# Kernel tuning notes

Measured on AMD Instinct MI355X. Metric: run time of the kernel, lower is better.

Reference implementation:

```python
import jax, jax.numpy as jnp
import numpy as np

B, T, V, S_FIXED, DIM, CV = 4, 256, 1024, 64, 1024, 256


def setup_inputs() -> dict:
    key = jax.random.key(0)
    ks = jax.random.split(key, 8)
    x = jax.random.normal(ks[0], (B, T, DIM), jnp.float32)
    vision = jax.random.normal(ks[1], (B, V, CV), jnp.float32)
    # attention mask (B, V, T): each text token t attends to exactly S_FIXED vision tokens
    scores = jax.random.uniform(ks[2], (B, T, V))
    _, sel = jax.lax.top_k(scores, S_FIXED)  # (B, T, S)
    mask_tv = jnp.zeros((B, T, V), bool)
    mask_tv = mask_tv.at[jnp.arange(B)[:, None, None], jnp.arange(T)[None, :, None], sel].set(True)
    attention_mask = jnp.transpose(mask_tv, (0, 2, 1))  # (B, V, T)
    # xavier-uniform-like params (scale irrelevant for correctness baseline)
    Wu = jax.random.normal(ks[3], (CV, DIM), jnp.float32) * (1.0 / np.sqrt(CV))
    bu = jax.random.normal(ks[4], (DIM,), jnp.float32) * 0.02
    Wk = jax.random.normal(ks[5], (DIM, DIM), jnp.float32) * (1.0 / np.sqrt(DIM))
    Wv = jax.random.normal(ks[6], (DIM, DIM), jnp.float32) * (1.0 / np.sqrt(DIM))
    return {"x": x, "vision": vision, "attention_mask": attention_mask,
            "Wu": Wu, "bu": bu, "Wk": Wk, "Wv": Wv, "S": S_FIXED}


def reference(x, vision, attention_mask, Wu, bu, Wk, Wv, S):
    Bv, Vn, Cv = vision.shape
    Bx, Tn, C = x.shape  # C == dim
    # --- _construct_sparse_inputs ---
    mask_tv = jnp.transpose(attention_mask, (0, 2, 1))  # (B, T, V)
    idx_full = jnp.where(mask_tv, jnp.arange(Vn, dtype=jnp.int32), jnp.int32(Vn))
    # topk(largest=False) == smallest S indices, ascending; pad value = Vn
    index = -jax.lax.top_k(-idx_full, S)[0]  # (B, T, S)
    vision_pad = jnp.concatenate([vision, jnp.zeros((Bv, 1, Cv), vision.dtype)], axis=1)  # (B, V+1, Cv)
    vg = jnp.take_along_axis(vision_pad, index.reshape(Bv, Tn * S, 1), axis=1)
    vg = vg.reshape(Bv, Tn, S, Cv)  # (B, T, S, 256)
    # NOTE: faithful to source — VALID positions receive the -100 bias
    mask_qk = (index != Vn)[..., None].astype(jnp.float32) * (-100.0)  # (B, T, S, 1)
    # --- attention ---
    vu = vg @ Wu + bu           # (B, T, S, dim)
    k = vu @ Wk                 # (B, T, S, dim)
    v = vu @ Wv                 # (B, T, S, dim)
    q = x[:, :, None, :]        # (B, T, 1, dim)
    qk = jnp.einsum('bksc,bktc->bkst', k, q) / jnp.sqrt(jnp.float32(C)) + mask_qk  # (B, T, S, 1)
    sm = jax.nn.softmax(qk.reshape(Bx, -1), axis=-1).reshape(qk.shape)  # softmax over flattened T*S*1
    attn = jnp.einsum('bkst,bksc->bktc', sm, v)  # (B, T, 1, dim)
    return (attn + q).squeeze(2)  # (B, T, dim)
```

## Files before the change

### kernel.cpp

```cpp
#include <hip/hip_runtime.h>
#include <stdint.h>

#define B 4
#define T 256
#define V 1024
#define S 64
#define DIM 1024
#define CV 256

typedef __attribute__((ext_vector_type(8))) short bf16x8;
typedef __attribute__((ext_vector_type(4))) short s16x4;
typedef __attribute__((ext_vector_type(4))) float f32x4;

enum : int {
    WKT_O   = 0,
    WVT_O   = WKT_O + 262144,
    WUB_O   = WVT_O + 262144,
    WKPB_O  = WUB_O + 131072,
    WVPT_O  = WKPB_O + 131072,
    XB_O    = WVPT_O + 131072,
    ZB_O    = XB_O + 262144,
    VB_O    = ZB_O + 131072,
    WB_O    = VB_O + 524288,
    RS_O    = WB_O + 131072,
    PIDX_O  = RS_O + B*T,
    BK_O    = PIDX_O + B*T*S,
    BV_O    = BK_O + DIM,
    BP_O    = BV_O + DIM,
    WS_TOTAL= BP_O + 2*16*1024
};

__device__ __forceinline__ short f2bf(float f) {
    union { float f; unsigned u; } x; x.f = f;
    unsigned r = (x.u + 0x7FFF + ((x.u >> 16) & 1)) >> 16;
    return (short)r;
}
__device__ __forceinline__ float bf2f(short s) {
    union { unsigned u; float f; } x;
    x.u = ((unsigned)(unsigned short)s) << 16;
    return x.f;
}
__device__ __forceinline__ s16x4 cvt4(float4 f) {
    s16x4 o;
    o.x = f2bf(f.x); o.y = f2bf(f.y); o.z = f2bf(f.z); o.w = f2bf(f.w);
    return o;
}

__global__ void stage1(const float* __restrict__ vision, const float* __restrict__ Wu,
                       const float* __restrict__ x, const float* __restrict__ Wk,
                       const float* __restrict__ Wv, const float* __restrict__ bu,
                       const void* __restrict__ maskp,
                       float* __restrict__ ws, int* __restrict__ wsi) {
    __shared__ short tlds[64 * 65];
    __shared__ float tred[4 * 64];
    __shared__ int mc_cnt[16][17];
    __shared__ int sa_flag, sb_flag;
    int blk = blockIdx.x;
    int tid = threadIdx.x;

    if (blk < 2304) {
        const float* src; short* dst; int idx;
        if (blk < 1024)      { src = vision; dst = (short*)(ws + VB_O);  idx = blk; }
        else if (blk < 1280) { src = Wu;     dst = (short*)(ws + WUB_O); idx = blk - 1024; }
        else                 { src = x;      dst = (short*)(ws + XB_O);  idx = blk - 1280; }
        int i = (idx * 256 + tid);
        ((s16x4*)dst)[i] = cvt4(((const float4*)src)[i]);
        return;
    }
    if (blk < 2816) {
        int tile = blk - 2304;
        int which = tile >> 8, t2 = tile & 255;
        int e0 = (t2 >> 4) * 64, d0 = (t2 & 15) * 64;
        const float* src = which ? Wv : Wk;
        short* dst = (short*)(ws + (which ? WVT_O : WKT_O));
        int j = tid & 63, i0 = tid >> 6;
        float pb = 0.f;
#pragma unroll
        for (int p = 0; p < 16; p++) {
            int i = p * 4 + i0;
            float v = src[(size_t)(e0 + i) * DIM + d0 + j];
            tlds[j * 65 + i] = f2bf(v);
            pb += bu[e0 + i] * v;
        }
        tred[i0 * 64 + j] = pb;
        __syncthreads();
#pragma unroll
        for (int p = 0; p < 16; p++) {
            int dd = p * 4 + i0;
            dst[(size_t)(d0 + dd) * DIM + e0 + j] = tlds[dd * 65 + j];
        }
        if (i0 == 0) {
            float s = tred[j] + tred[64 + j] + tred[128 + j] + tred[192 + j];
            ws[BP_O + (which * 16 + (e0 >> 6)) * 1024 + d0 + j] = s;
        }
        return;
    }
    {
        int a = 0, bfl = 0;
        const uchar4* m4 = (const uchar4*)maskp;
#pragma unroll
        for (int jj = 0; jj < 4; jj++) {
            uchar4 u = m4[tid * 4 + jj];
            if (u.y | u.z | u.w) a = 1;
            if (u.x == 0x3f || u.y == 0x3f || u.z == 0x3f || u.w == 0x3f) bfl = 1;
        }
        if (tid == 0) { sa_flag = 0; sb_flag = 0; }
        __syncthreads();
        if (a) sa_flag = 1;
        if (bfl) sb_flag = 1;
        __syncthreads();
    }
    bool byteMode = sa_flag && !sb_flag;
    int mb = blk - 2816;
    int b = mb >> 4, tg = mb & 15;
    int tl = tid & 15, c = tid >> 4;
    int t = tg * 16 + tl;
    int v0 = c * 64;
    unsigned long long bits = 0ull;
    if (byteMode) {
        const uint8_t* m = (const uint8_t*)maskp + (size_t)(b * V + v0) * T + t;
#pragma unroll 8
        for (int j = 0; j < 64; j++)
            if (m[(size_t)j * T] != 0) bits |= 1ull << j;
    } else {
        const int* m = (const int*)maskp + (size_t)(b * V + v0) * T + t;
#pragma unroll 8
        for (int j = 0; j < 64; j++)
            if (m[(size_t)j * T] != 0) bits |= 1ull << j;
    }
    mc_cnt[tl][c] = __popcll(bits);
    __syncthreads();
    int off = 0, total = 0;
#pragma unroll
    for (int cc = 0; cc < 16; cc++) {
        int cn = mc_cnt[tl][cc];
        if (cc < c) off += cn;
        total += cn;
    }
    int base = PIDX_O + (b * T + t) * S;
    while (bits) {
        int j = __ffsll(bits) - 1;
        bits &= bits - 1;
        if (off < S) wsi[base + off] = v0 + j;
        off++;
    }
    if (c == 15)
        for (int j = (total < S ? total : S); j < S; j++) wsi[base + j] = 0;
}

template<int K, int LDA, int LDB>
__device__ __forceinline__ void wave_mma(const short* __restrict__ A0,
                                         const short* __restrict__ B0,
                                         f32x4 acc[2][2]) {
    int lane = threadIdx.x & 63;
    int rw = lane & 15, q = lane >> 4;
    const short* ap0 = A0 + rw * LDA + q * 8;
    const short* ap1 = ap0 + 16 * LDA;
    const short* bp0 = B0 + rw * LDB + q * 8;
    const short* bp1 = bp0 + 16 * LDB;
#pragma unroll 4
    for (int kc = 0; kc < K; kc += 32) {
        bf16x8 a0 = *(const bf16x8*)(ap0 + kc);
        bf16x8 a1 = *(const bf16x8*)(ap1 + kc);
        bf16x8 b0 = *(const bf16x8*)(bp0 + kc);
        bf16x8 b1 = *(const bf16x8*)(bp1 + kc);
        acc[0][0] = __builtin_amdgcn_mfma_f32_16x16x32_bf16(a0, b0, acc[0][0], 0, 0, 0);
        acc[0][1] = __builtin_amdgcn_mfma_f32_16x16x32_bf16(a0, b1, acc[0][1], 0, 0, 0);
        acc[1][0] = __builtin_amdgcn_mfma_f32_16x16x32_bf16(a1, b0, acc[1][0], 0, 0, 0);
        acc[1][1] = __builtin_amdgcn_mfma_f32_16x16x32_bf16(a1, b1, acc[1][1], 0, 0, 0);
    }
}

__device__ __forceinline__ bool splitk_reduce(f32x4 acc[2][2],
                                              float (*red)[64][17],
                                              int wv, int lane) {
    if (wv > 0) {
#pragma unroll
        for (int i = 0; i < 2; i++)
#pragma unroll
            for (int j = 0; j < 2; j++)
#pragma unroll
                for (int r = 0; r < 4; r++)
                    red[wv - 1][lane][(i * 2 + j) * 4 + r] = acc[i][j][r];
    }
    __syncthreads();
    if (wv != 0) return false;
#pragma unroll
    for (int i = 0; i < 2; i++)
#pragma unroll
        for (int j = 0; j < 2; j++)
#pragma unroll
            for (int r = 0; r < 4; r++) {
                int c = (i * 2 + j) * 4 + r;
                acc[i][j][r] += red[0][lane][c] + red[1][lane][c] + red[2][lane][c];
            }
    return true;
}

__global__ void g_prep_mfma(float* __restrict__ ws) {
    if (blockIdx.x >= 512) {
        int which = blockIdx.x - 512;
#pragma unroll
        for (int cch = 0; cch < 4; cch++) {
            int d = cch * 256 + threadIdx.x;
            float s = 0.f;
#pragma unroll
            for (int g = 0; g < 16; g++)
                s += ws[BP_O + (which * 16 + g) * 1024 + d];
            ws[(which ? BV_O : BK_O) + d] = s;
        }
        return;
    }
    __shared__ float red[3][64][17];
    int tile = blockIdx.x;
    int which = tile >> 8, rem = tile & 255;
    int m0 = (rem >> 5) * 32, n0 = (rem & 31) * 32;
    int wv = threadIdx.x >> 6, lane = threadIdx.x & 63;
    const short* A = (const short*)(ws + WUB_O) + (size_t)m0 * DIM + wv * 256;
    const short* Bt = (const short*)(ws + (which ? WVT_O : WKT_O)) + (size_t)n0 * DIM + wv * 256;
    f32x4 acc[2][2] = {};
    wave_mma<256, DIM, DIM>(A, Bt, acc);
    if (!splitk_reduce(acc, red, wv, lane)) return;
    int col = lane & 15, q = lane >> 4;
    if (which == 0) {
        short* o = (short*)(ws + WKPB_O);
#pragma unroll
        for (int i = 0; i < 2; i++)
#pragma unroll
            for (int j = 0; j < 2; j++)
#pragma unroll
                for (int r = 0; r < 4; r++)
                    o[(size_t)(m0 + i * 16 + q * 4 + r) * DIM + n0 + j * 16 + col] =
                        f2bf(acc[i][j][r]);
    } else {
        short* o = (short*)(ws + WVPT_O);
#pragma unroll
        for (int i = 0; i < 2; i++)
#pragma unroll
            for (int j = 0; j < 2; j++) {
                s16x4 v;
                v.x = f2bf(acc[i][j][0]); v.y = f2bf(acc[i][j][1]);
                v.z = f2bf(acc[i][j][2]); v.w = f2bf(acc[i][j][3]);
                *(s16x4*)&o[(size_t)(n0 + j * 16 + col) * CV + m0 + i * 16 + q * 4] = v;
            }
    }
}

__global__ void g_z_mfma(float* __restrict__ ws) {
    __shared__ float red[3][64][17];
    int w = blockIdx.x;
    int m0 = (w >> 3) * 32, n0 = (w & 7) * 32;
    int wv = threadIdx.x >> 6, lane = threadIdx.x & 63;
    const short* A = (const short*)(ws + XB_O) + (size_t)m0 * DIM + wv * 256;
    const short* Bt = (const short*)(ws + WKPB_O) + (size_t)n0 * DIM + wv * 256;
    f32x4 acc[2][2] = {};
    wave_mma<256, DIM, DIM>(A, Bt, acc);
    if (!splitk_reduce(acc, red, wv, lane)) return;
    int col = lane & 15, q = lane >> 4;
    short* zb = (short*)(ws + ZB_O);
#pragma unroll
    for (int i = 0; i < 2; i++)
#pragma unroll
        for (int j = 0; j < 2; j++)
#pragma unroll
            for (int r = 0; r < 4; r++)
                zb[(size_t)(m0 + i * 16 + q * 4 + r) * CV + n0 + j * 16 + col] =
                    f2bf(acc[i][j][r]);
}

__global__ void __launch_bounds__(256, 4)
g_attn(const float* __restrict__ x, float* __restrict__ ws,
       int* __restrict__ wsi) {
    __shared__ short svr[64 * 256];
    __shared__ int   s_idx[64];
    __shared__ float s_sc[64];
    __shared__ float s_c0[4];
    __shared__ float s_wa[3][64][5];
    int tid = threadIdx.x;
    int lane = tid & 63, wv = tid >> 6;
    int blk = blockIdx.x;
    int bt = ((blk & 7) << 7) + (blk >> 3);
    int b = bt >> 8;

    if (tid < 64) s_idx[tid] = wsi[PIDX_O + bt * S + tid];
    {
        const float4* xr = (const float4*)(x + (size_t)bt * DIM);
        const float4* bkr = (const float4*)(ws + BK_O);
        float4 a = xr[wv * 64 + lane], k4 = bkr[wv * 64 + lane];
        float c0p = a.x * k4.x + a.y * k4.y + a.z * k4.z + a.w * k4.w;
        for (int o = 32; o > 0; o >>= 1) c0p += __shfl_xor(c0p, o);
        if (lane == 0) s_c0[wv] = c0p;
    }
    __syncthreads();
    const short* vb = (const short*)(ws + VB_O) + (size_t)b * V * CV;
    {
        int r = tid >> 2, part = tid & 3;
        const bf16x8* src = (const bf16x8*)(vb + (size_t)s_idx[r] * CV);
#pragma unroll
        for (int i = 0; i < 8; i++) {
            int c = part * 8 + i;
            int sl = c ^ (r & 7);
            *(bf16x8*)((char*)svr + r * 512 + sl * 16) = src[c];
        }
    }
    __syncthreads();
    int rw = lane & 15, q = lane >> 4;
    {
        const short* zp = (const short*)(ws + ZB_O) + (size_t)bt * CV + q * 8;
        int srow = wv * 16 + rw;
        f32x4 a4 = {0.f, 0.f, 0.f, 0.f};
#pragma unroll
        for (int kc8 = 0; kc8 < 8; kc8++) {
            int sl = (q + kc8 * 4) ^ (srow & 7);
            bf16x8 av = *(const bf16x8*)((char*)svr + srow * 512 + sl * 16);
            bf16x8 bv = *(const bf16x8*)(zp + kc8 * 32);
            a4 = __builtin_amdgcn_mfma_f32_16x16x32_bf16(av, bv, a4, 0, 0, 0);
        }
        if (rw == 0) {
#pragma unroll
            for (int r = 0; r < 4; r++)
                s_sc[wv * 16 + q * 4 + r] = a4[r];
        }
    }
    __syncthreads();
    float c0 = s_c0[0] + s_c0[1] + s_c0[2] + s_c0[3];
    float p = expf((s_sc[lane] + c0) * 0.03125f);
    float rs = p;
    for (int o = 32; o > 0; o >>= 1) rs += __shfl_xor(rs, o);
    if (tid == 0) ws[RS_O + bt] = rs;
    float4 wa = {0.f, 0.f, 0.f, 0.f};
#pragma unroll
    for (int si = 0; si < 16; si++) {
        int s = wv * 16 + si;
        float pv = __shfl(p, s);
        int sl = (lane >> 1) ^ (s & 7);
        s16x4 r4 = *(const s16x4*)((char*)svr + s * 512 + sl * 16 + (lane & 1) * 8);
        wa.x += pv * bf2f(r4.x); wa.y += pv * bf2f(r4.y);
        wa.z += pv * bf2f(r4.z); wa.w += pv * bf2f(r4.w);
    }
    if (wv > 0) {
        s_wa[wv - 1][lane][0] = wa.x; s_wa[wv - 1][lane][1] = wa.y;
        s_wa[wv - 1][lane][2] = wa.z; s_wa[wv - 1][lane][3] = wa.w;
    }
    __syncthreads();
    if (wv == 0) {
#pragma unroll
        for (int g = 0; g < 3; g++) {
            wa.x += s_wa[g][lane][0]; wa.y += s_wa[g][lane][1];
            wa.z += s_wa[g][lane][2]; wa.w += s_wa[g][lane][3];
        }
        s16x4 o;
        o.x = f2bf(wa.x); o.y = f2bf(wa.y); o.z = f2bf(wa.z); o.w = f2bf(wa.w);
        ((s16x4*)((short*)(ws + WB_O) + (size_t)bt * CV))[lane] = o;
    }
}

__global__ void g_out_mfma(const float* __restrict__ x, float* __restrict__ ws,
                           float* __restrict__ out) {
    int w = blockIdx.x * 4 + (threadIdx.x >> 6);
    int m0 = (w >> 6) * 32, n0 = (w & 63) * 16;
    int lane = threadIdx.x & 63;
    int b = m0 >> 8;
    float4 r4 = *(const float4*)(ws + RS_O + b * 256 + lane * 4);
    float dn = r4.x + r4.y + r4.z + r4.w;
    for (int o = 32; o > 0; o >>= 1) dn += __shfl_xor(dn, o);
    float inv = 1.0f / dn;
    int rw = lane & 15, q = lane >> 4;
    const short* A  = (const short*)(ws + WB_O)   + (size_t)m0 * CV;
    const short* Bt = (const short*)(ws + WVPT_O) + (size_t)n0 * CV;
    const short* ap0 = A + rw * CV + q * 8;
    const short* ap1 = ap0 + 16 * CV;
    const short* bp0 = Bt + rw * CV + q * 8;
    f32x4 acc[2] = {};
#pragma unroll 4
    for (int kc = 0; kc < CV; kc += 32) {
        bf16x8 a0 = *(const bf16x8*)(ap0 + kc);
        bf16x8 a1 = *(const bf16x8*)(ap1 + kc);
        bf16x8 b0 = *(const bf16x8*)(bp0 + kc);
        acc[0] = __builtin_amdgcn_mfma_f32_16x16x32_bf16(a0, b0, acc[0], 0, 0, 0);
        acc[1] = __builtin_amdgcn_mfma_f32_16x16x32_bf16(a1, b0, acc[1], 0, 0, 0);
    }
    int col = lane & 15;
#pragma unroll
    for (int i = 0; i < 2; i++)
#pragma unroll
        for (int r = 0; r < 4; r++) {
            int row = m0 + i * 16 + q * 4 + r;
            float rs = ws[RS_O + row];
            int cc = n0 + col;
            out[(size_t)row * DIM + cc] =
                x[(size_t)row * DIM + cc] +
                (acc[i][r] + rs * ws[BV_O + cc]) * inv;
        }
}

extern "C" void kernel_launch(void* const* d_in, const int* in_sizes, int n_in,
                              void* d_out, int out_size, void* d_ws, size_t ws_size,
                              hipStream_t stream) {
    (void)in_sizes; (void)n_in; (void)out_size; (void)ws_size;
    const float* x      = (const float*)d_in[0];
    const float* vision = (const float*)d_in[1];
    const void*  mask   = d_in[2];
    const float* Wu     = (const float*)d_in[3];
    const float* bu     = (const float*)d_in[4];
    const float* Wk     = (const float*)d_in[5];
    const float* Wv     = (const float*)d_in[6];
    float* out = (float*)d_out;
    float* ws  = (float*)d_ws;
    int*   wsi = (int*)d_ws;

    stage1<<<2880, 256, 0, stream>>>(vision, Wu, x, Wk, Wv, bu, mask, ws, wsi);
    g_prep_mfma<<<514, 256, 0, stream>>>(ws);
    g_z_mfma<<<256, 256, 0, stream>>>(ws);
    g_attn<<<1024, 256, 0, stream>>>(x, ws, wsi);
    g_out_mfma<<<512, 256, 0, stream>>>(x, ws, out);
}
```

Baseline: 116.5 us.

## Rebalance weight-product and Z GEMMs across kernels with 8-way split-K

```diff
diff --git a/kernel.cpp b/kernel.cpp
--- a/kernel.cpp
+++ b/kernel.cpp
@@ -158,7 +158,7 @@
     const short* ap1 = ap0 + 16 * LDA;
     const short* bp0 = B0 + rw * LDB + q * 8;
     const short* bp1 = bp0 + 16 * LDB;
-#pragma unroll 4
+#pragma unroll
     for (int kc = 0; kc < K; kc += 32) {
         bf16x8 a0 = *(const bf16x8*)(ap0 + kc);
         bf16x8 a1 = *(const bf16x8*)(ap1 + kc);
@@ -171,9 +171,9 @@
     }
 }
 
-__device__ __forceinline__ bool splitk_reduce(f32x4 acc[2][2],
-                                              float (*red)[64][17],
-                                              int wv, int lane) {
+__device__ __forceinline__ bool splitk_reduce8(f32x4 acc[2][2],
+                                               float (*red)[64][17],
+                                               int wv, int lane) {
     if (wv > 0) {
 #pragma unroll
         for (int i = 0; i < 2; i++)
@@ -192,47 +192,74 @@
 #pragma unroll
             for (int r = 0; r < 4; r++) {
                 int c = (i * 2 + j) * 4 + r;
-                acc[i][j][r] += red[0][lane][c] + red[1][lane][c] + red[2][lane][c];
+                float s = acc[i][j][r];
+#pragma unroll
+                for (int g = 0; g < 7; g++) s += red[g][lane][c];
+                acc[i][j][r] = s;
             }
     return true;
 }
 
-__global__ void g_prep_mfma(float* __restrict__ ws) {
-    if (blockIdx.x >= 512) {
-        int which = blockIdx.x - 512;
-#pragma unroll
-        for (int cch = 0; cch < 4; cch++) {
-            int d = cch * 256 + threadIdx.x;
+__global__ void __launch_bounds__(512, 2)
+g_wkp(float* __restrict__ ws) {
+    if (blockIdx.x >= 256) {
+#pragma unroll
+        for (int cch = 0; cch < 2; cch++) {
+            int d = cch * 512 + threadIdx.x;
             float s = 0.f;
 #pragma unroll
             for (int g = 0; g < 16; g++)
-                s += ws[BP_O + (which * 16 + g) * 1024 + d];
-            ws[(which ? BV_O : BK_O) + d] = s;
+                s += ws[BP_O + g * 1024 + d];
+            ws[BK_O + d] = s;
         }
         return;
     }
-    __shared__ float red[3][64][17];
-    int tile = blockIdx.x;
-    int which = tile >> 8, rem = tile & 255;
+    __shared__ float red[7][64][17];
+    int rem = blockIdx.x;
     int m0 = (rem >> 5) * 32, n0 = (rem & 31) * 32;
     int wv = threadIdx.x >> 6, lane = threadIdx.x & 63;
-    const short* A = (const short*)(ws + WUB_O) + (size_t)m0 * DIM + wv * 256;
-    const short* Bt = (const short*)(ws + (which ? WVT_O : WKT_O)) + (size_t)n0 * DIM + wv * 256;
+    const short* A  = (const short*)(ws + WUB_O) + (size_t)m0 * DIM + wv * 128;
+    const short* Bt = (const short*)(ws + WKT_O) + (size_t)n0 * DIM + wv * 128;
     f32x4 acc[2][2] = {};
-    wave_mma<256, DIM, DIM>(A, Bt, acc);
-    if (!splitk_reduce(acc, red, wv, lane)) return;
+    wave_mma<128, DIM, DIM>(A, Bt, acc);
+    if (!splitk_reduce8(acc, red, wv, lane)) return;
     int col = lane & 15, q = lane >> 4;
-    if (which == 0) {
-        short* o = (short*)(ws + WKPB_O);
-#pragma unroll
-        for (int i = 0; i < 2; i++)
-#pragma unroll
-            for (int j = 0; j < 2; j++)
-#pragma unroll
-                for (int r = 0; r < 4; r++)
-                    o[(size_t)(m0 + i * 16 + q * 4 + r) * DIM + n0 + j * 16 + col] =
-                        f2bf(acc[i][j][r]);
-    } else {
+    short* o = (short*)(ws + WKPB_O);
+#pragma unroll
+    for (int i = 0; i < 2; i++)
+#pragma unroll
+        for (int j = 0; j < 2; j++)
+#pragma unroll
+            for (int r = 0; r < 4; r++)
+                o[(size_t)(m0 + i * 16 + q * 4 + r) * DIM + n0 + j * 16 + col] =
+                    f2bf(acc[i][j][r]);
+}
+
+__global__ void __launch_bounds__(512, 2)
+g_wvp_z(float* __restrict__ ws) {
+    if (blockIdx.x >= 512) {
+#pragma unroll
+        for (int cch = 0; cch < 2; cch++) {
+            int d = cch * 512 + threadIdx.x;
+            float s = 0.f;
+#pragma unroll
+            for (int g = 0; g < 16; g++)
+                s += ws[BP_O + (16 + g) * 1024 + d];
+            ws[BV_O + d] = s;
+        }
+        return;
+    }
+    __shared__ float red[7][64][17];
+    int wv = threadIdx.x >> 6, lane = threadIdx.x & 63;
+    if (blockIdx.x < 256) {
+        int rem = blockIdx.x;
+        int m0 = (rem >> 5) * 32, n0 = (rem & 31) * 32;
+        const short* A  = (const short*)(ws + WUB_O) + (size_t)m0 * DIM + wv * 128;
+        const short* Bt = (const short*)(ws + WVT_O) + (size_t)n0 * DIM + wv * 128;
+        f32x4 acc[2][2] = {};
+        wave_mma<128, DIM, DIM>(A, Bt, acc);
+        if (!splitk_reduce8(acc, red, wv, lane)) return;
+        int col = lane & 15, q = lane >> 4;
         short* o = (short*)(ws + WVPT_O);
 #pragma unroll
         for (int i = 0; i < 2; i++)
@@ -243,29 +270,25 @@
                 v.z = f2bf(acc[i][j][2]); v.w = f2bf(acc[i][j][3]);
                 *(s16x4*)&o[(size_t)(n0 + j * 16 + col) * CV + m0 + i * 16 + q * 4] = v;
             }
-    }
-}
-
-__global__ void g_z_mfma(float* __restrict__ ws) {
-    __shared__ float red[3][64][17];
-    int w = blockIdx.x;
-    int m0 = (w >> 3) * 32, n0 = (w & 7) * 32;
-    int wv = threadIdx.x >> 6, lane = threadIdx.x & 63;
-    const short* A = (const short*)(ws + XB_O) + (size_t)m0 * DIM + wv * 256;
-    const short* Bt = (const short*)(ws + WKPB_O) + (size_t)n0 * DIM + wv * 256;
-    f32x4 acc[2][2] = {};
-    wave_mma<256, DIM, DIM>(A, Bt, acc);
-    if (!splitk_reduce(acc, red, wv, lane)) return;
-    int col = lane & 15, q = lane >> 4;
-    short* zb = (short*)(ws + ZB_O);
-#pragma unroll
-    for (int i = 0; i < 2; i++)
-#pragma unroll
-        for (int j = 0; j < 2; j++)
-#pragma unroll
-            for (int r = 0; r < 4; r++)
-                zb[(size_t)(m0 + i * 16 + q * 4 + r) * CV + n0 + j * 16 + col] =
-                    f2bf(acc[i][j][r]);
+    } else {
+        int rem = blockIdx.x - 256;
+        int m0 = (rem >> 3) * 32, n0 = (rem & 7) * 32;
+        const short* A  = (const short*)(ws + XB_O)   + (size_t)m0 * DIM + wv * 128;
+        const short* Bt = (const short*)(ws + WKPB_O) + (size_t)n0 * DIM + wv * 128;
+        f32x4 acc[2][2] = {};
+        wave_mma<128, DIM, DIM>(A, Bt, acc);
+        if (!splitk_reduce8(acc, red, wv, lane)) return;
+        int col = lane & 15, q = lane >> 4;
+        short* zb = (short*)(ws + ZB_O);
+#pragma unroll
+        for (int i = 0; i < 2; i++)
+#pragma unroll
+            for (int j = 0; j < 2; j++)
+#pragma unroll
+                for (int r = 0; r < 4; r++)
+                    zb[(size_t)(m0 + i * 16 + q * 4 + r) * CV + n0 + j * 16 + col] =
+                        f2bf(acc[i][j][r]);
+    }
 }
 
 __global__ void __launch_bounds__(256, 4)
@@ -410,8 +433,8 @@
     int*   wsi = (int*)d_ws;
 
     stage1<<<2880, 256, 0, stream>>>(vision, Wu, x, Wk, Wv, bu, mask, ws, wsi);
-    g_prep_mfma<<<514, 256, 0, stream>>>(ws);
-    g_z_mfma<<<256, 256, 0, stream>>>(ws);
+    g_wkp<<<257, 512, 0, stream>>>(ws);
+    g_wvp_z<<<513, 512, 0, stream>>>(ws);
     g_attn<<<1024, 256, 0, stream>>>(x, ws, wsi);
     g_out_mfma<<<512, 256, 0, stream>>>(x, ws, out);
 }
```

After: 116.0 us. Within noise of the previous version (-0.4%).
